# Kernel tuning notes

Hardware: AMD Instinct MI355X
Metric: run time of the kernel (lower is better)

Reference implementation:

```python
import jax, jax.numpy as jnp
import numpy as np

N = 100000
E = 600000
H = 128
OUT = 64
L = 3

def glorot(key, shape):
    fan_in, fan_out = shape[0], shape[1]
    lim = jnp.sqrt(6.0 / (fan_in + fan_out))
    return jax.random.uniform(key, shape, jnp.float32, -lim, lim)

def setup_inputs() -> dict:
    key = jax.random.key(0)
    ks = jax.random.split(key, 20)
    x = jax.random.normal(ks[0], (N, H), jnp.float32)
    edge_index = jax.random.randint(ks[1], (2, E), 0, N, jnp.int64)
    edge_attr = jax.random.uniform(ks[2], (E, 1), jnp.float32)
    # stacked per-layer params [L, ...]
    W_lin = jnp.stack([glorot(jax.random.fold_in(ks[3], i), (H, H)) for i in range(L)])
    b_lin = jnp.zeros((L, H), jnp.float32)
    W_msg = jnp.stack([glorot(jax.random.fold_in(ks[4], i), (H + 1, H)) for i in range(L)])
    b_msg = jnp.zeros((L, H), jnp.float32)
    W_l = jnp.stack([glorot(jax.random.fold_in(ks[5], i), (H, H)) for i in range(L)])
    b_l = jnp.zeros((L, H), jnp.float32)
    W_r = jnp.stack([glorot(jax.random.fold_in(ks[6], i), (H, H)) for i in range(L)])
    W_dec = glorot(ks[7], (H, H))
    b_dec = jnp.zeros((H,), jnp.float32)
    W_fin = glorot(ks[8], (H, OUT))
    b_fin = jnp.zeros((OUT,), jnp.float32)
    return {"x": x, "edge_attr": edge_attr, "W_lin": W_lin, "b_lin": b_lin,
            "W_msg": W_msg, "b_msg": b_msg, "W_l": W_l, "b_l": b_l, "W_r": W_r,
            "W_dec": W_dec, "b_dec": b_dec, "W_fin": W_fin, "b_fin": b_fin,
            "edge_index": edge_index}

def reference(x, edge_attr, W_lin, b_lin, W_msg, b_msg, W_l, b_l, W_r,
              W_dec, b_dec, W_fin, b_fin, edge_index):
    src, dst = edge_index[0], edge_index[1]  # j -> i (source_to_target)
    # mean-aggregation denominator: in-degree clamped to 1
    deg = jax.ops.segment_sum(jnp.ones((E,), jnp.float32), dst, num_segments=N)
    inv_deg = (1.0 / jnp.maximum(deg, 1.0))[:, None]  # [N,1]
    for l in range(L):
        h = jax.nn.relu(x @ W_lin[l] + b_lin[l])          # [N,H]
        msg_in = jnp.concatenate([h[src], edge_attr], -1)  # [E,H+1]
        msg = jax.nn.relu(msg_in @ W_msg[l] + b_msg[l])    # [E,H]
        agg = jax.ops.segment_sum(msg, dst, num_segments=N) * inv_deg  # [N,H]
        out = (agg @ W_l[l] + b_l[l]) + x @ W_r[l]         # lin_l(agg) + lin_r(x_r)
        x = jax.nn.relu(out)  # dropout p=0.0 -> identity
    emb = jax.nn.relu(x @ W_dec + b_dec)
    logits = emb @ W_fin + b_fin  # [N,OUT]
    return logits
```

## Files before the change

### kernel.cpp

```cpp
#include <hip/hip_runtime.h>

using short8 = __attribute__((ext_vector_type(8))) short;
using f32x4  = __attribute__((ext_vector_type(4))) float;

constexpr int HD = 128;
constexpr int NBLK_SCAT = 4096;

__device__ __forceinline__ unsigned short f2bf(float f) {
    unsigned u = __builtin_bit_cast(unsigned, f);
    u += 0x7fffu + ((u >> 16) & 1u);
    return (unsigned short)(u >> 16);
}
__device__ __forceinline__ float bflo(unsigned u) { return __builtin_bit_cast(float, u << 16); }
__device__ __forceinline__ float bfhi(unsigned u) { return __builtin_bit_cast(float, u & 0xffff0000u); }

__device__ __forceinline__ short8 ldg8(const unsigned short* p) {
    return *reinterpret_cast<const short8*>(p);
}

__device__ __forceinline__ void dev_chain(unsigned short* As1, unsigned short* Hs,
    const unsigned short* __restrict__ A, const unsigned short* __restrict__ Wt1,
    const unsigned short* __restrict__ Wtc, const float* __restrict__ b1,
    const float* __restrict__ b2, unsigned short* __restrict__ Out, int nrows, int bid)
{
    const int tid  = threadIdx.x;
    const int lane = tid & 63, wave = tid >> 6;
    const int lr = lane & 15, lg = lane >> 4;
    const int row0 = bid * 64;

#pragma unroll
    for (int it = 0; it < 4; ++it) {
        const int q   = wave * 4 + it;
        const int c   = q * 64 + lane;
        const int row = c >> 4, cw = c & 15;
        int grow = row0 + row; grow = grow < nrows ? grow : nrows - 1;
        const int gco = (cw ^ (row & 7)) << 3;
        __builtin_amdgcn_global_load_lds((const unsigned int*)(A + (long)grow * HD + gco),
                                         (unsigned int*)&As1[q * 512], 16, 0, 0);
    }

    const int cb = wave * 32;
    short8 bf1[2][4];
#pragma unroll
    for (int ct = 0; ct < 2; ++ct) {
        const unsigned short* bp = Wt1 + (long)(cb + ct * 16 + lr) * HD + lg * 8;
#pragma unroll
        for (int kt = 0; kt < 4; ++kt) bf1[ct][kt] = ldg8(bp + kt * 32);
    }
    short8 bfc[2][4];
#pragma unroll
    for (int ct = 0; ct < 2; ++ct) {
        const unsigned short* bp = Wtc + (long)(cb + ct * 16 + lr) * HD + lg * 8;
#pragma unroll
        for (int kt = 0; kt < 4; ++kt) bfc[ct][kt] = ldg8(bp + kt * 32);
    }

    __syncthreads();

    f32x4 acc[4][2] = {};
#pragma unroll
    for (int kt = 0; kt < 4; ++kt) {
        short8 af[4];
#pragma unroll
        for (int rt = 0; rt < 4; ++rt)
            af[rt] = *reinterpret_cast<const short8*>(
                &As1[(rt * 16 + lr) * HD + (((kt * 4 + lg) ^ (lr & 7)) << 3)]);
#pragma unroll
        for (int rt = 0; rt < 4; ++rt)
#pragma unroll
            for (int ct = 0; ct < 2; ++ct)
                acc[rt][ct] = __builtin_amdgcn_mfma_f32_16x16x32_bf16(af[rt], bf1[ct][kt], acc[rt][ct], 0, 0, 0);
    }

    const float bv1[2] = { b1[cb + lr], b1[cb + 16 + lr] };
#pragma unroll
    for (int rt = 0; rt < 4; ++rt)
#pragma unroll
        for (int ct = 0; ct < 2; ++ct) {
            const int cc = cb + ct * 16 + lr;
#pragma unroll
            for (int i = 0; i < 4; ++i) {
                const int row = rt * 16 + lg * 4 + i;
                const float v = fmaxf(acc[rt][ct][i] + bv1[ct], 0.f);
                Hs[row * HD + ((((cc >> 3) ^ (row & 7)) << 3) | (cc & 7))] = f2bf(v);
            }
        }
    __syncthreads();

    f32x4 acc2[4][2] = {};
#pragma unroll
    for (int kt = 0; kt < 4; ++kt) {
        short8 ah[4];
#pragma unroll
        for (int rt = 0; rt < 4; ++rt)
            ah[rt] = *reinterpret_cast<const short8*>(
                &Hs[(rt * 16 + lr) * HD + (((kt * 4 + lg) ^ (lr & 7)) << 3)]);
#pragma unroll
        for (int rt = 0; rt < 4; ++rt)
#pragma unroll
            for (int ct = 0; ct < 2; ++ct)
                acc2[rt][ct] = __builtin_amdgcn_mfma_f32_16x16x32_bf16(ah[rt], bfc[ct][kt], acc2[rt][ct], 0, 0, 0);
    }
    const float bv2[2] = { b2[cb + lr], b2[cb + 16 + lr] };
#pragma unroll
    for (int rt = 0; rt < 4; ++rt)
#pragma unroll
        for (int ct = 0; ct < 2; ++ct) {
            const int cc = cb + ct * 16 + lr;
#pragma unroll
            for (int i = 0; i < 4; ++i) {
                const int row = rt * 16 + lg * 4 + i;
                As1[row * HD + ((((cc >> 3) ^ (row & 7)) << 3) | (cc & 7))] = f2bf(acc2[rt][ct][i] + bv2[ct]);
            }
        }
    __syncthreads();

#pragma unroll
    for (int k = 0; k < 4; ++k) {
        const int c   = tid + k * 256;
        const int row = c >> 4, cw = c & 15;
        const int r = row0 + row;
        if (r < nrows) {
            const uint4 v = *reinterpret_cast<const uint4*>(
                &As1[row * HD + ((cw ^ (row & 7)) << 3)]);
            *reinterpret_cast<uint4*>(Out + (long)r * HD + cw * 8) = v;
        }
    }
}

__global__ __launch_bounds__(256)
void k_dualchain(const unsigned short* __restrict__ Agg, const unsigned short* __restrict__ X,
                 const unsigned short* __restrict__ WtL, const unsigned short* __restrict__ WtR,
                 const float* __restrict__ bl_,
                 const unsigned short* __restrict__ Wt1, const float* __restrict__ b1,
                 const unsigned short* __restrict__ Wtc, const float* __restrict__ b2,
                 unsigned short* __restrict__ Xout, unsigned short* __restrict__ Gout, int n)
{
    __shared__ __align__(16) unsigned short Ag[64 * HD];
    __shared__ __align__(16) unsigned short Xs[64 * HD];
    __shared__ __align__(16) unsigned short Ts[64 * HD];

    const int tid  = threadIdx.x;
    const int lane = tid & 63, wave = tid >> 6;
    const int lr = lane & 15, lg = lane >> 4;
    const int row0 = blockIdx.x * 64;

#pragma unroll
    for (int it = 0; it < 4; ++it) {
        const int q   = wave * 4 + it;
        const int c   = q * 64 + lane;
        const int row = c >> 4, cw = c & 15;
        int grow = row0 + row; grow = grow < n ? grow : n - 1;
        const int gco = (cw ^ (row & 7)) << 3;
        __builtin_amdgcn_global_load_lds((const unsigned int*)(Agg + (long)grow * HD + gco),
                                         (unsigned int*)&Ag[q * 512], 16, 0, 0);
        __builtin_amdgcn_global_load_lds((const unsigned int*)(X + (long)grow * HD + gco),
                                         (unsigned int*)&Xs[q * 512], 16, 0, 0);
    }

    const int cb = wave * 32;
    short8 bl[2][4], br[2][4];
#pragma unroll
    for (int ct = 0; ct < 2; ++ct) {
        const unsigned short* pl = WtL + (long)(cb + ct * 16 + lr) * HD + lg * 8;
        const unsigned short* pr = WtR + (long)(cb + ct * 16 + lr) * HD + lg * 8;
#pragma unroll
        for (int kt = 0; kt < 4; ++kt) { bl[ct][kt] = ldg8(pl + kt * 32); br[ct][kt] = ldg8(pr + kt * 32); }
    }
    __syncthreads();

    {
        f32x4 acc[4][2] = {};
#pragma unroll
        for (int kt = 0; kt < 4; ++kt) {
            short8 aa[4], ax[4];
#pragma unroll
            for (int rt = 0; rt < 4; ++rt) {
                const int base = (rt * 16 + lr) * HD + (((kt * 4 + lg) ^ (lr & 7)) << 3);
                aa[rt] = *reinterpret_cast<const short8*>(&Ag[base]);
                ax[rt] = *reinterpret_cast<const short8*>(&Xs[base]);
            }
#pragma unroll
            for (int rt = 0; rt < 4; ++rt)
#pragma unroll
                for (int ct = 0; ct < 2; ++ct) {
                    acc[rt][ct] = __builtin_amdgcn_mfma_f32_16x16x32_bf16(aa[rt], bl[ct][kt], acc[rt][ct], 0, 0, 0);
                    acc[rt][ct] = __builtin_amdgcn_mfma_f32_16x16x32_bf16(ax[rt], br[ct][kt], acc[rt][ct], 0, 0, 0);
                }
        }
        const float bv[2] = { bl_[cb + lr], bl_[cb + 16 + lr] };
#pragma unroll
        for (int rt = 0; rt < 4; ++rt)
#pragma unroll
            for (int ct = 0; ct < 2; ++ct) {
                const int cc = cb + ct * 16 + lr;
#pragma unroll
                for (int i = 0; i < 4; ++i) {
                    const int row = rt * 16 + lg * 4 + i;
                    const float v = fmaxf(acc[rt][ct][i] + bv[ct], 0.f);
                    Ts[row * HD + ((((cc >> 3) ^ (row & 7)) << 3) | (cc & 7))] = f2bf(v);
                }
            }
    }
    __syncthreads();

    {
        short8 b1f[2][4];
#pragma unroll
        for (int ct = 0; ct < 2; ++ct) {
            const unsigned short* bp = Wt1 + (long)(cb + ct * 16 + lr) * HD + lg * 8;
#pragma unroll
            for (int kt = 0; kt < 4; ++kt) b1f[ct][kt] = ldg8(bp + kt * 32);
        }
        f32x4 a2[4][2] = {};
#pragma unroll
        for (int kt = 0; kt < 4; ++kt) {
            short8 ah[4];
#pragma unroll
            for (int rt = 0; rt < 4; ++rt)
                ah[rt] = *reinterpret_cast<const short8*>(
                    &Ts[(rt * 16 + lr) * HD + (((kt * 4 + lg) ^ (lr & 7)) << 3)]);
#pragma unroll
            for (int rt = 0; rt < 4; ++rt)
#pragma unroll
                for (int ct = 0; ct < 2; ++ct)
                    a2[rt][ct] = __builtin_amdgcn_mfma_f32_16x16x32_bf16(ah[rt], b1f[ct][kt], a2[rt][ct], 0, 0, 0);
        }
        short8 bcf[2][4];
#pragma unroll
        for (int ct = 0; ct < 2; ++ct) {
            const unsigned short* bp = Wtc + (long)(cb + ct * 16 + lr) * HD + lg * 8;
#pragma unroll
            for (int kt = 0; kt < 4; ++kt) bcf[ct][kt] = ldg8(bp + kt * 32);
        }
        const float bv[2] = { b1[cb + lr], b1[cb + 16 + lr] };
#pragma unroll
        for (int rt = 0; rt < 4; ++rt)
#pragma unroll
            for (int ct = 0; ct < 2; ++ct) {
                const int cc = cb + ct * 16 + lr;
#pragma unroll
                for (int i = 0; i < 4; ++i) {
                    const int row = rt * 16 + lg * 4 + i;
                    const float v = fmaxf(a2[rt][ct][i] + bv[ct], 0.f);
                    Ag[row * HD + ((((cc >> 3) ^ (row & 7)) << 3) | (cc & 7))] = f2bf(v);
                }
            }
        __syncthreads();

        f32x4 a3[4][2] = {};
#pragma unroll
        for (int kt = 0; kt < 4; ++kt) {
            short8 ah[4];
#pragma unroll
            for (int rt = 0; rt < 4; ++rt)
                ah[rt] = *reinterpret_cast<const short8*>(
                    &Ag[(rt * 16 + lr) * HD + (((kt * 4 + lg) ^ (lr & 7)) << 3)]);
#pragma unroll
            for (int rt = 0; rt < 4; ++rt)
#pragma unroll
                for (int ct = 0; ct < 2; ++ct)
                    a3[rt][ct] = __builtin_amdgcn_mfma_f32_16x16x32_bf16(ah[rt], bcf[ct][kt], a3[rt][ct], 0, 0, 0);
        }
        const float bv2[2] = { b2[cb + lr], b2[cb + 16 + lr] };
#pragma unroll
        for (int rt = 0; rt < 4; ++rt)
#pragma unroll
            for (int ct = 0; ct < 2; ++ct) {
                const int cc = cb + ct * 16 + lr;
#pragma unroll
                for (int i = 0; i < 4; ++i) {
                    const int row = rt * 16 + lg * 4 + i;
                    Xs[row * HD + ((((cc >> 3) ^ (row & 7)) << 3) | (cc & 7))] = f2bf(a3[rt][ct][i] + bv2[ct]);
                }
            }
    }
    __syncthreads();

#pragma unroll
    for (int k = 0; k < 4; ++k) {
        const int c   = tid + k * 256;
        const int row = c >> 4, cw = c & 15;
        const int r = row0 + row;
        if (r < n) {
            const int off = row * HD + ((cw ^ (row & 7)) << 3);
            *reinterpret_cast<uint4*>(Xout + (long)r * HD + cw * 8) =
                *reinterpret_cast<const uint4*>(&Ts[off]);
            *reinterpret_cast<uint4*>(Gout + (long)r * HD + cw * 8) =
                *reinterpret_cast<const uint4*>(&Xs[off]);
        }
    }
}

__global__ __launch_bounds__(256)
void k_dualdec(const unsigned short* __restrict__ Agg, const unsigned short* __restrict__ X,
               const unsigned short* __restrict__ WtL, const unsigned short* __restrict__ WtR,
               const float* __restrict__ bl_, const unsigned short* __restrict__ Wdec,
               const float* __restrict__ bdec, const unsigned short* __restrict__ Wfin,
               const float* __restrict__ bfin, float* __restrict__ Out, int n)
{
    __shared__ __align__(16) unsigned short Ag[64 * HD];
    __shared__ __align__(16) unsigned short Xs[64 * HD];
    __shared__ __align__(16) unsigned short Ts[64 * HD];

    const int tid  = threadIdx.x;
    const int lane = tid & 63, wave = tid >> 6;
    const int lr = lane & 15, lg = lane >> 4;
    const int row0 = blockIdx.x * 64;

#pragma unroll
    for (int it = 0; it < 4; ++it) {
        const int q   = wave * 4 + it;
        const int c   = q * 64 + lane;
        const int row = c >> 4, cw = c & 15;
        int grow = row0 + row; grow = grow < n ? grow : n - 1;
        const int gco = (cw ^ (row & 7)) << 3;
        __builtin_amdgcn_global_load_lds((const unsigned int*)(Agg + (long)grow * HD + gco),
                                         (unsigned int*)&Ag[q * 512], 16, 0, 0);
        __builtin_amdgcn_global_load_lds((const unsigned int*)(X + (long)grow * HD + gco),
                                         (unsigned int*)&Xs[q * 512], 16, 0, 0);
    }

    const int cb = wave * 32;
    short8 bl[2][4], br[2][4];
#pragma unroll
    for (int ct = 0; ct < 2; ++ct) {
        const unsigned short* pl = WtL + (long)(cb + ct * 16 + lr) * HD + lg * 8;
        const unsigned short* pr = WtR + (long)(cb + ct * 16 + lr) * HD + lg * 8;
#pragma unroll
        for (int kt = 0; kt < 4; ++kt) { bl[ct][kt] = ldg8(pl + kt * 32); br[ct][kt] = ldg8(pr + kt * 32); }
    }
    __syncthreads();

    {
        f32x4 acc[4][2] = {};
#pragma unroll
        for (int kt = 0; kt < 4; ++kt) {
            short8 aa[4], ax[4];
#pragma unroll
            for (int rt = 0; rt < 4; ++rt) {
                const int base = (rt * 16 + lr) * HD + (((kt * 4 + lg) ^ (lr & 7)) << 3);
                aa[rt] = *reinterpret_cast<const short8*>(&Ag[base]);
                ax[rt] = *reinterpret_cast<const short8*>(&Xs[base]);
            }
#pragma unroll
            for (int rt = 0; rt < 4; ++rt)
#pragma unroll
                for (int ct = 0; ct < 2; ++ct) {
                    acc[rt][ct] = __builtin_amdgcn_mfma_f32_16x16x32_bf16(aa[rt], bl[ct][kt], acc[rt][ct], 0, 0, 0);
                    acc[rt][ct] = __builtin_amdgcn_mfma_f32_16x16x32_bf16(ax[rt], br[ct][kt], acc[rt][ct], 0, 0, 0);
                }
        }
        const float bv[2] = { bl_[cb + lr], bl_[cb + 16 + lr] };
#pragma unroll
        for (int rt = 0; rt < 4; ++rt)
#pragma unroll
            for (int ct = 0; ct < 2; ++ct) {
                const int cc = cb + ct * 16 + lr;
#pragma unroll
                for (int i = 0; i < 4; ++i) {
                    const int row = rt * 16 + lg * 4 + i;
                    const float v = fmaxf(acc[rt][ct][i] + bv[ct], 0.f);
                    Ts[row * HD + ((((cc >> 3) ^ (row & 7)) << 3) | (cc & 7))] = f2bf(v);
                }
            }
    }
    __syncthreads();

    {
        short8 bd[2][4];
#pragma unroll
        for (int ct = 0; ct < 2; ++ct) {
            const unsigned short* bp = Wdec + (long)(cb + ct * 16 + lr) * HD + lg * 8;
#pragma unroll
            for (int kt = 0; kt < 4; ++kt) bd[ct][kt] = ldg8(bp + kt * 32);
        }
        f32x4 a2[4][2] = {};
#pragma unroll
        for (int kt = 0; kt < 4; ++kt) {
            short8 ah[4];
#pragma unroll
            for (int rt = 0; rt < 4; ++rt)
                ah[rt] = *reinterpret_cast<const short8*>(
                    &Ts[(rt * 16 + lr) * HD + (((kt * 4 + lg) ^ (lr & 7)) << 3)]);
#pragma unroll
            for (int rt = 0; rt < 4; ++rt)
#pragma unroll
                for (int ct = 0; ct < 2; ++ct)
                    a2[rt][ct] = __builtin_amdgcn_mfma_f32_16x16x32_bf16(ah[rt], bd[ct][kt], a2[rt][ct], 0, 0, 0);
        }
        const int cbf = wave * 16;
        short8 bfn[4];
#pragma unroll
        for (int kt = 0; kt < 4; ++kt)
            bfn[kt] = ldg8(Wfin + (long)(cbf + lr) * HD + lg * 8 + kt * 32);
        const float bv[2] = { bdec[cb + lr], bdec[cb + 16 + lr] };
#pragma unroll
        for (int rt = 0; rt < 4; ++rt)
#pragma unroll
            for (int ct = 0; ct < 2; ++ct) {
                const int cc = cb + ct * 16 + lr;
#pragma unroll
                for (int i = 0; i < 4; ++i) {
                    const int row = rt * 16 + lg * 4 + i;
                    const float v = fmaxf(a2[rt][ct][i] + bv[ct], 0.f);
                    Ag[row * HD + ((((cc >> 3) ^ (row & 7)) << 3) | (cc & 7))] = f2bf(v);
                }
            }
        __syncthreads();

        f32x4 a3[4] = {};
#pragma unroll
        for (int kt = 0; kt < 4; ++kt) {
            short8 ah[4];
#pragma unroll
            for (int rt = 0; rt < 4; ++rt)
                ah[rt] = *reinterpret_cast<const short8*>(
                    &Ag[(rt * 16 + lr) * HD + (((kt * 4 + lg) ^ (lr & 7)) << 3)]);
#pragma unroll
            for (int rt = 0; rt < 4; ++rt)
                a3[rt] = __builtin_amdgcn_mfma_f32_16x16x32_bf16(ah[rt], bfn[kt], a3[rt], 0, 0, 0);
        }
        const float bvf = bfin[cbf + lr];
#pragma unroll
        for (int rt = 0; rt < 4; ++rt)
#pragma unroll
            for (int i = 0; i < 4; ++i) {
                const int r = row0 + rt * 16 + lg * 4 + i;
                if (r < n) Out[(long)r * 64 + cbf + lr] = a3[rt][i] + bvf;
            }
    }
}

__device__ __forceinline__ void dev_deg(const int* __restrict__ dst, int* __restrict__ deg,
                                        int nE, int n, int bid, int nblk) {
    const int grp = bid & 7, bin = bid >> 3, nbin = nblk >> 3;
    const int chunk = (n + 7) >> 3;
    const int lo = grp * chunk, hi = min(n, lo + chunk);
    for (int e = bin * 256 + threadIdx.x; e < nE; e += nbin * 256) {
        const int d = dst[e];
        if (d >= lo && d < hi) atomicAdd(&deg[d], 1);
    }
}

__global__ __launch_bounds__(256)
void k_fill(const int* __restrict__ src, const int* __restrict__ dst,
            const float* __restrict__ eattr, const int* __restrict__ rowstart,
            int* __restrict__ degcur, uint2* __restrict__ csr_rec, int nE, int n)
{
    const int bid = blockIdx.x, nblk = gridDim.x;
    const int grp = bid & 7, bin = bid >> 3, nbin = nblk >> 3;
    const int chunk = (n + 7) >> 3;
    const int lo = grp * chunk, hi = min(n, lo + chunk);
    for (int e = bin * 256 + threadIdx.x; e < nE; e += nbin * 256) {
        const int d = dst[e];
        if (d >= lo && d < hi) {
            const int p = rowstart[d] + atomicSub(&degcur[d], 1) - 1;
            uint2 rec;
            rec.x = (unsigned)src[e];
            rec.y = __builtin_bit_cast(unsigned, eattr[e]);
            csr_rec[p] = rec;
        }
    }
}

__global__ __launch_bounds__(256)
void k_u1(const int* __restrict__ dst, int* __restrict__ deg, int nE,
          const float* __restrict__ xin, unsigned short* __restrict__ xb, long n8, int ncast,
          const float* __restrict__ Wlin, const float* __restrict__ Wmsg,
          const float* __restrict__ Wl,   const float* __restrict__ Wr,
          const float* __restrict__ Wdec, const float* __restrict__ Wfin,
          unsigned short* __restrict__ wt, int n)
{
    const int bid = blockIdx.x;
    if (bid < NBLK_SCAT) { dev_deg(dst, deg, nE, n, bid, NBLK_SCAT); return; }
    const int b = bid - NBLK_SCAT;
    if (b < ncast) {
        const long i = (long)b * 256 + threadIdx.x;
        if (i >= n8) return;
        const float4 v0 = *((const float4*)xin + i * 2);
        const float4 v1 = *((const float4*)xin + i * 2 + 1);
        unsigned o[4];
        o[0] = (unsigned)f2bf(v0.x) | ((unsigned)f2bf(v0.y) << 16);
        o[1] = (unsigned)f2bf(v0.z) | ((unsigned)f2bf(v0.w) << 16);
        o[2] = (unsigned)f2bf(v1.x) | ((unsigned)f2bf(v1.y) << 16);
        o[3] = (unsigned)f2bf(v1.z) | ((unsigned)f2bf(v1.w) << 16);
        *(uint4*)(xb + i * 8) = *(uint4*)o;
        return;
    }
    const int local = b - ncast;
    const int m = local >> 6;
    const float* src; int C = 128;
    if      (m < 3)  src = Wlin + m * 16384;
    else if (m < 6)  src = Wmsg + (m - 3) * (129 * 128);
    else if (m < 9)  src = Wl   + (m - 6) * 16384;
    else if (m < 12) src = Wr   + (m - 9) * 16384;
    else if (m == 12) src = Wdec;
    else { src = Wfin; C = 64; }
    const int elems = C * 128;
    const int e = (local & 63) * 256 + threadIdx.x;
    if (e >= elems) return;
    const int c = e >> 7, k = e & 127;
    wt[m * 16384 + e] = f2bf(src[k * C + c]);
}

__global__ __launch_bounds__(256)
void k_u2(const int* __restrict__ deg, int* __restrict__ csum, int nch,
          const unsigned short* __restrict__ A, const unsigned short* __restrict__ Wt1,
          const unsigned short* __restrict__ Wtc, const float* __restrict__ b1,
          const float* __restrict__ b2, unsigned short* __restrict__ Out, int n)
{
    __shared__ __align__(16) unsigned short As1[64 * HD];
    __shared__ __align__(16) unsigned short Hs [64 * HD];
    if ((int)blockIdx.x < nch) {
        __shared__ int s[256];
        const int t = threadIdx.x, i = blockIdx.x * 256 + t;
        s[t] = (i < n) ? deg[i] : 0;
        __syncthreads();
        for (int o = 128; o > 0; o >>= 1) { if (t < o) s[t] += s[t + o]; __syncthreads(); }
        if (t == 0) csum[blockIdx.x] = s[0];
        return;
    }
    dev_chain(As1, Hs, A, Wt1, Wtc, b1, b2, Out, n, blockIdx.x - nch);
}

__global__ void k_scanmid(const int* __restrict__ csum, int* __restrict__ cbase,
                          int* __restrict__ rowstart, int nch, int n) {
    __shared__ int s[512];
    int t = threadIdx.x;
    int v = (t < nch) ? csum[t] : 0;
    s[t] = v; __syncthreads();
    for (int off = 1; off < 512; off <<= 1) {
        int tmp = (t >= off) ? s[t - off] : 0;
        __syncthreads();
        s[t] += tmp;
        __syncthreads();
    }
    if (t < nch) cbase[t] = s[t] - v;
    if (t == nch - 1) rowstart[n] = s[t];
}

__global__ void k_scan2(const int* __restrict__ deg, const int* __restrict__ cbase,
                        int* __restrict__ rowstart, float* __restrict__ inv_deg, int n) {
    __shared__ int s[256];
    int t = threadIdx.x, i = blockIdx.x * 256 + t;
    int v = (i < n) ? deg[i] : 0;
    s[t] = v; __syncthreads();
    for (int off = 1; off < 256; off <<= 1) {
        int tmp = (t >= off) ? s[t - off] : 0;
        __syncthreads();
        s[t] += tmp;
        __syncthreads();
    }
    if (i < n) {
        rowstart[i] = cbase[blockIdx.x] + s[t] - v;
        inv_deg[i] = 1.0f / fmaxf((float)v, 1.0f);
    }
}

__global__ __launch_bounds__(256)
void k_agg(const unsigned short* __restrict__ g, const uint2* __restrict__ rec,
           const int* __restrict__ rs, const float* __restrict__ inv_deg,
           const float* __restrict__ wlast, unsigned short* __restrict__ agg, int n) {
    const int lane = threadIdx.x & 15;
    const int node = blockIdx.x * 16 + (threadIdx.x >> 4);
    if (node >= n) return;
    const int c0 = lane * 8;
    const float4 wla = *(const float4*)(wlast + c0);
    const float4 wlb = *(const float4*)(wlast + c0 + 4);
    const int p0 = rs[node], p1 = rs[node + 1];
    float a0=0,a1=0,a2=0,a3=0,a4=0,a5=0,a6=0,a7=0;
    int p = p0;
    for (; p + 4 <= p1; p += 4) {
        uint2 r[4];
#pragma unroll
        for (int u = 0; u < 4; ++u) r[u] = rec[p + u];
        uint4 G[4];
#pragma unroll
        for (int u = 0; u < 4; ++u) G[u] = *(const uint4*)(g + (long)r[u].x * HD + c0);
#pragma unroll
        for (int u = 0; u < 4; ++u) {
            const float e = __builtin_bit_cast(float, r[u].y);
            a0 += fmaxf(fmaf(e, wla.x, bflo(G[u].x)), 0.f);
            a1 += fmaxf(fmaf(e, wla.y, bfhi(G[u].x)), 0.f);
            a2 += fmaxf(fmaf(e, wla.z, bflo(G[u].y)), 0.f);
            a3 += fmaxf(fmaf(e, wla.w, bfhi(G[u].y)), 0.f);
            a4 += fmaxf(fmaf(e, wlb.x, bflo(G[u].z)), 0.f);
            a5 += fmaxf(fmaf(e, wlb.y, bfhi(G[u].z)), 0.f);
            a6 += fmaxf(fmaf(e, wlb.z, bflo(G[u].w)), 0.f);
            a7 += fmaxf(fmaf(e, wlb.w, bfhi(G[u].w)), 0.f);
        }
    }
    for (; p < p1; ++p) {
        const uint2 r0 = rec[p];
        const float e0 = __builtin_bit_cast(float, r0.y);
        const uint4 G0 = *(const uint4*)(g + (long)r0.x * HD + c0);
        a0 += fmaxf(fmaf(e0, wla.x, bflo(G0.x)), 0.f);
        a1 += fmaxf(fmaf(e0, wla.y, bfhi(G0.x)), 0.f);
        a2 += fmaxf(fmaf(e0, wla.z, bflo(G0.y)), 0.f);
        a3 += fmaxf(fmaf(e0, wla.w, bfhi(G0.y)), 0.f);
        a4 += fmaxf(fmaf(e0, wlb.x, bflo(G0.z)), 0.f);
        a5 += fmaxf(fmaf(e0, wlb.y, bfhi(G0.z)), 0.f);
        a6 += fmaxf(fmaf(e0, wlb.z, bflo(G0.w)), 0.f);
        a7 += fmaxf(fmaf(e0, wlb.w, bfhi(G0.w)), 0.f);
    }
    const float id = inv_deg[node];
    uint4 o;
    o.x = (unsigned)f2bf(a0 * id) | ((unsigned)f2bf(a1 * id) << 16);
    o.y = (unsigned)f2bf(a2 * id) | ((unsigned)f2bf(a3 * id) << 16);
    o.z = (unsigned)f2bf(a4 * id) | ((unsigned)f2bf(a5 * id) << 16);
    o.w = (unsigned)f2bf(a6 * id) | ((unsigned)f2bf(a7 * id) << 16);
    *(uint4*)(agg + (long)node * HD + c0) = o;
}

extern "C" void kernel_launch(void* const* d_in, const int* in_sizes, int n_in,
                              void* d_out, int out_size, void* d_ws, size_t ws_size,
                              hipStream_t stream)
{
    const float* x     = (const float*)d_in[0];
    const float* eattr = (const float*)d_in[1];
    const float* W_lin = (const float*)d_in[2];
    const float* b_lin = (const float*)d_in[3];
    const float* W_msg = (const float*)d_in[4];
    const float* b_msg = (const float*)d_in[5];
    const float* W_l   = (const float*)d_in[6];
    const float* b_l   = (const float*)d_in[7];
    const float* W_r   = (const float*)d_in[8];
    const float* W_dec = (const float*)d_in[9];
    const float* b_dec = (const float*)d_in[10];
    const float* W_fin = (const float*)d_in[11];
    const float* b_fin = (const float*)d_in[12];
    const int*   ei    = (const int*)d_in[13];

    const int N = in_sizes[0] / HD;
    const int E = in_sizes[1];
    const int* srcv = ei;
    const int* dstv = ei + E;

    char* wsb = (char*)d_ws;
    size_t off = 0;
    auto carve = [&](size_t bytes) -> void* {
        void* p = wsb + off;
        off += (bytes + 255) & ~(size_t)255;
        return p;
    };
    unsigned short* xb = (unsigned short*)carve((size_t)N * HD * 2);
    unsigned short* t1 = (unsigned short*)carve((size_t)N * HD * 2);
    unsigned short* t2 = (unsigned short*)carve((size_t)N * HD * 2);
    unsigned short* t3 = (unsigned short*)carve((size_t)N * HD * 2);
    unsigned short* wt = (unsigned short*)carve((size_t)14 * 16384 * 2);
    uint2* csr_rec  = (uint2*)carve((size_t)E * 8);
    int*   rowstart = (int*)carve((size_t)(N + 1) * 4);
    int*   deg      = (int*)carve((size_t)N * 4);
    float* inv_deg  = (float*)carve((size_t)N * 4);
    const int NCH = (N + 255) / 256;
    int* csum  = (int*)carve((size_t)NCH * 4);
    int* cbase = (int*)carve((size_t)NCH * 4);

    if (off > ws_size) {
        hipMemsetAsync(d_out, 0, (size_t)out_size * 4, stream);
        return;
    }

    hipMemsetAsync(deg, 0, (size_t)N * 4, stream);

    auto WT = [&](int m) { return wt + (size_t)m * 16384; };
    const int NB64 = (N + 63) / 64;
    const int GAGG = (N + 15) / 16;
    const long n8 = (long)N * HD / 8;
    const int ncast = (int)((n8 + 255) / 256);

    k_u1<<<NBLK_SCAT + ncast + 14 * 64, 256, 0, stream>>>(
        dstv, deg, E, x, xb, n8, ncast, W_lin, W_msg, W_l, W_r, W_dec, W_fin, wt, N);
    k_u2<<<NCH + NB64, 256, 0, stream>>>(
        deg, csum, NCH, xb, WT(0), WT(3), b_lin, b_msg, t2, N);
    k_scanmid<<<1, 512, 0, stream>>>(csum, cbase, rowstart, NCH, N);
    k_scan2<<<NCH, 256, 0, stream>>>(deg, cbase, rowstart, inv_deg, N);
    k_fill<<<NBLK_SCAT, 256, 0, stream>>>(srcv, dstv, eattr, rowstart, deg, csr_rec, E, N);

    auto wlast = [&](int l) { return W_msg + (size_t)l * (HD + 1) * HD + (size_t)HD * HD; };

    k_agg<<<GAGG, 256, 0, stream>>>(t2, csr_rec, rowstart, inv_deg, wlast(0), t1, N);
    k_dualchain<<<NB64, 256, 0, stream>>>(
        t1, xb, WT(6), WT(9), b_l, WT(1), b_lin + HD, WT(4), b_msg + HD, t3, t2, N);
    k_agg<<<GAGG, 256, 0, stream>>>(t2, csr_rec, rowstart, inv_deg, wlast(1), t1, N);
    k_dualchain<<<NB64, 256, 0, stream>>>(
        t1, t3, WT(7), WT(10), b_l + HD, WT(2), b_lin + 2 * HD, WT(5), b_msg + 2 * HD, xb, t2, N);
    k_agg<<<GAGG, 256, 0, stream>>>(t2, csr_rec, rowstart, inv_deg, wlast(2), t1, N);
    k_dualdec<<<NB64, 256, 0, stream>>>(t1, xb, WT(8), WT(11), b_l + 2 * HD,
                                        WT(12), b_dec, WT(13), b_fin, (float*)d_out, N);
}
```

Measured before the change: 300.8 us.

## Split fused dual-chain kernel into separate dual and chain kernels

Replaces the fused k_dualchain kernel with two launches per layer: k_dual computes the layer update and writes the new node features, and k_chain reads them back to compute the next layer's lin and message transforms. This lowers shared memory per block from three tiles to two, which may allow higher occupancy. The cost is an extra global write and read of the node feature matrix plus one more kernel launch per layer.

```diff
diff --git a/kernel.cpp b/kernel.cpp
--- a/kernel.cpp
+++ b/kernel.cpp
@@ -129,16 +129,22 @@
 }
 
 __global__ __launch_bounds__(256)
-void k_dualchain(const unsigned short* __restrict__ Agg, const unsigned short* __restrict__ X,
-                 const unsigned short* __restrict__ WtL, const unsigned short* __restrict__ WtR,
-                 const float* __restrict__ bl_,
-                 const unsigned short* __restrict__ Wt1, const float* __restrict__ b1,
-                 const unsigned short* __restrict__ Wtc, const float* __restrict__ b2,
-                 unsigned short* __restrict__ Xout, unsigned short* __restrict__ Gout, int n)
+void k_chain(const unsigned short* __restrict__ A, const unsigned short* __restrict__ Wt1,
+             const unsigned short* __restrict__ Wtc, const float* __restrict__ b1,
+             const float* __restrict__ b2, unsigned short* __restrict__ Out, int nrows)
+{
+    __shared__ __align__(16) unsigned short As1[64 * HD];
+    __shared__ __align__(16) unsigned short Hs [64 * HD];
+    dev_chain(As1, Hs, A, Wt1, Wtc, b1, b2, Out, nrows, blockIdx.x);
+}
+
+__global__ __launch_bounds__(256)
+void k_dual(const unsigned short* __restrict__ Agg, const unsigned short* __restrict__ X,
+            const unsigned short* __restrict__ WtL, const unsigned short* __restrict__ WtR,
+            const float* __restrict__ bl_, unsigned short* __restrict__ Xout, int n)
 {
     __shared__ __align__(16) unsigned short Ag[64 * HD];
     __shared__ __align__(16) unsigned short Xs[64 * HD];
-    __shared__ __align__(16) unsigned short Ts[64 * HD];
 
     const int tid  = threadIdx.x;
     const int lane = tid & 63, wave = tid >> 6;
@@ -169,112 +175,39 @@
     }
     __syncthreads();
 
-    {
-        f32x4 acc[4][2] = {};
-#pragma unroll
-        for (int kt = 0; kt < 4; ++kt) {
-            short8 aa[4], ax[4];
-#pragma unroll
-            for (int rt = 0; rt < 4; ++rt) {
-                const int base = (rt * 16 + lr) * HD + (((kt * 4 + lg) ^ (lr & 7)) << 3);
-                aa[rt] = *reinterpret_cast<const short8*>(&Ag[base]);
-                ax[rt] = *reinterpret_cast<const short8*>(&Xs[base]);
-            }
-#pragma unroll
-            for (int rt = 0; rt < 4; ++rt)
-#pragma unroll
-                for (int ct = 0; ct < 2; ++ct) {
-                    acc[rt][ct] = __builtin_amdgcn_mfma_f32_16x16x32_bf16(aa[rt], bl[ct][kt], acc[rt][ct], 0, 0, 0);
-                    acc[rt][ct] = __builtin_amdgcn_mfma_f32_16x16x32_bf16(ax[rt], br[ct][kt], acc[rt][ct], 0, 0, 0);
-                }
-        }
-        const float bv[2] = { bl_[cb + lr], bl_[cb + 16 + lr] };
+    f32x4 acc[4][2] = {};
+#pragma unroll
+    for (int kt = 0; kt < 4; ++kt) {
+        short8 aa[4], ax[4];
+#pragma unroll
+        for (int rt = 0; rt < 4; ++rt) {
+            const int base = (rt * 16 + lr) * HD + (((kt * 4 + lg) ^ (lr & 7)) << 3);
+            aa[rt] = *reinterpret_cast<const short8*>(&Ag[base]);
+            ax[rt] = *reinterpret_cast<const short8*>(&Xs[base]);
+        }
 #pragma unroll
         for (int rt = 0; rt < 4; ++rt)
 #pragma unroll
             for (int ct = 0; ct < 2; ++ct) {
-                const int cc = cb + ct * 16 + lr;
-#pragma unroll
-                for (int i = 0; i < 4; ++i) {
-                    const int row = rt * 16 + lg * 4 + i;
-                    const float v = fmaxf(acc[rt][ct][i] + bv[ct], 0.f);
-                    Ts[row * HD + ((((cc >> 3) ^ (row & 7)) << 3) | (cc & 7))] = f2bf(v);
-                }
-            }
-    }
-    __syncthreads();
-
-    {
-        short8 b1f[2][4];
+                acc[rt][ct] = __builtin_amdgcn_mfma_f32_16x16x32_bf16(aa[rt], bl[ct][kt], acc[rt][ct], 0, 0, 0);
+                acc[rt][ct] = __builtin_amdgcn_mfma_f32_16x16x32_bf16(ax[rt], br[ct][kt], acc[rt][ct], 0, 0, 0);
+            }
+    }
+    __syncthreads();
+
+    const float bv[2] = { bl_[cb + lr], bl_[cb + 16 + lr] };
+#pragma unroll
+    for (int rt = 0; rt < 4; ++rt)
 #pragma unroll
         for (int ct = 0; ct < 2; ++ct) {
-            const unsigned short* bp = Wt1 + (long)(cb + ct * 16 + lr) * HD + lg * 8;
-#pragma unroll
-            for (int kt = 0; kt < 4; ++kt) b1f[ct][kt] = ldg8(bp + kt * 32);
-        }
-        f32x4 a2[4][2] = {};
-#pragma unroll
-        for (int kt = 0; kt < 4; ++kt) {
-            short8 ah[4];
-#pragma unroll
-            for (int rt = 0; rt < 4; ++rt)
-                ah[rt] = *reinterpret_cast<const short8*>(
-                    &Ts[(rt * 16 + lr) * HD + (((kt * 4 + lg) ^ (lr & 7)) << 3)]);
-#pragma unroll
-            for (int rt = 0; rt < 4; ++rt)
-#pragma unroll
-                for (int ct = 0; ct < 2; ++ct)
-                    a2[rt][ct] = __builtin_amdgcn_mfma_f32_16x16x32_bf16(ah[rt], b1f[ct][kt], a2[rt][ct], 0, 0, 0);
-        }
-        short8 bcf[2][4];
-#pragma unroll
-        for (int ct = 0; ct < 2; ++ct) {
-            const unsigned short* bp = Wtc + (long)(cb + ct * 16 + lr) * HD + lg * 8;
-#pragma unroll
-            for (int kt = 0; kt < 4; ++kt) bcf[ct][kt] = ldg8(bp + kt * 32);
-        }
-        const float bv[2] = { b1[cb + lr], b1[cb + 16 + lr] };
-#pragma unroll
-        for (int rt = 0; rt < 4; ++rt)
-#pragma unroll
-            for (int ct = 0; ct < 2; ++ct) {
-                const int cc = cb + ct * 16 + lr;
-#pragma unroll
-                for (int i = 0; i < 4; ++i) {
-                    const int row = rt * 16 + lg * 4 + i;
-                    const float v = fmaxf(a2[rt][ct][i] + bv[ct], 0.f);
-                    Ag[row * HD + ((((cc >> 3) ^ (row & 7)) << 3) | (cc & 7))] = f2bf(v);
-                }
-            }
-        __syncthreads();
-
-        f32x4 a3[4][2] = {};
-#pragma unroll
-        for (int kt = 0; kt < 4; ++kt) {
-            short8 ah[4];
-#pragma unroll
-            for (int rt = 0; rt < 4; ++rt)
-                ah[rt] = *reinterpret_cast<const short8*>(
-                    &Ag[(rt * 16 + lr) * HD + (((kt * 4 + lg) ^ (lr & 7)) << 3)]);
-#pragma unroll
-            for (int rt = 0; rt < 4; ++rt)
-#pragma unroll
-                for (int ct = 0; ct < 2; ++ct)
-                    a3[rt][ct] = __builtin_amdgcn_mfma_f32_16x16x32_bf16(ah[rt], bcf[ct][kt], a3[rt][ct], 0, 0, 0);
-        }
-        const float bv2[2] = { b2[cb + lr], b2[cb + 16 + lr] };
-#pragma unroll
-        for (int rt = 0; rt < 4; ++rt)
-#pragma unroll
-            for (int ct = 0; ct < 2; ++ct) {
-                const int cc = cb + ct * 16 + lr;
-#pragma unroll
-                for (int i = 0; i < 4; ++i) {
-                    const int row = rt * 16 + lg * 4 + i;
-                    Xs[row * HD + ((((cc >> 3) ^ (row & 7)) << 3) | (cc & 7))] = f2bf(a3[rt][ct][i] + bv2[ct]);
-                }
-            }
-    }
+            const int cc = cb + ct * 16 + lr;
+#pragma unroll
+            for (int i = 0; i < 4; ++i) {
+                const int row = rt * 16 + lg * 4 + i;
+                const float v = fmaxf(acc[rt][ct][i] + bv[ct], 0.f);
+                Ag[row * HD + ((((cc >> 3) ^ (row & 7)) << 3) | (cc & 7))] = f2bf(v);
+            }
+        }
     __syncthreads();
 
 #pragma unroll
@@ -283,11 +216,9 @@
         const int row = c >> 4, cw = c & 15;
         const int r = row0 + row;
         if (r < n) {
-            const int off = row * HD + ((cw ^ (row & 7)) << 3);
-            *reinterpret_cast<uint4*>(Xout + (long)r * HD + cw * 8) =
-                *reinterpret_cast<const uint4*>(&Ts[off]);
-            *reinterpret_cast<uint4*>(Gout + (long)r * HD + cw * 8) =
-                *reinterpret_cast<const uint4*>(&Xs[off]);
+            const uint4 v = *reinterpret_cast<const uint4*>(
+                &Ag[row * HD + ((cw ^ (row & 7)) << 3)]);
+            *reinterpret_cast<uint4*>(Xout + (long)r * HD + cw * 8) = v;
         }
     }
 }
@@ -681,11 +612,11 @@
     auto wlast = [&](int l) { return W_msg + (size_t)l * (HD + 1) * HD + (size_t)HD * HD; };
 
     k_agg<<<GAGG, 256, 0, stream>>>(t2, csr_rec, rowstart, inv_deg, wlast(0), t1, N);
-    k_dualchain<<<NB64, 256, 0, stream>>>(
-        t1, xb, WT(6), WT(9), b_l, WT(1), b_lin + HD, WT(4), b_msg + HD, t3, t2, N);
+    k_dual<<<NB64, 256, 0, stream>>>(t1, xb, WT(6), WT(9), b_l, t3, N);
+    k_chain<<<NB64, 256, 0, stream>>>(t3, WT(1), WT(4), b_lin + HD, b_msg + HD, t2, N);
     k_agg<<<GAGG, 256, 0, stream>>>(t2, csr_rec, rowstart, inv_deg, wlast(1), t1, N);
-    k_dualchain<<<NB64, 256, 0, stream>>>(
-        t1, t3, WT(7), WT(10), b_l + HD, WT(2), b_lin + 2 * HD, WT(5), b_msg + 2 * HD, xb, t2, N);
+    k_dual<<<NB64, 256, 0, stream>>>(t1, t3, WT(7), WT(10), b_l + HD, xb, N);
+    k_chain<<<NB64, 256, 0, stream>>>(xb, WT(2), WT(5), b_lin + 2 * HD, b_msg + 2 * HD, t2, N);
     k_agg<<<GAGG, 256, 0, stream>>>(t2, csr_rec, rowstart, inv_deg, wlast(2), t1, N);
     k_dualdec<<<NB64, 256, 0, stream>>>(t1, xb, WT(8), WT(11), b_l + 2 * HD,
                                         WT(12), b_dec, WT(13), b_fin, (float*)d_out, N);
```

Result: slower. 310.2 us (+3.1%).
